# Optimization experiments

Measured on AMD Instinct MI355X. Metric: run time of the kernel, lower is better.

Reference implementation:

```python
import jax, jax.numpy as jnp
import numpy as np


def setup_inputs() -> dict:
    key = jax.random.key(0)
    k1, k2 = jax.random.split(key)
    x = jax.random.normal(k1, (8, 8192, 512), dtype=jnp.float32)
    codebook = jax.random.normal(k2, (1024, 512), dtype=jnp.float32)
    return {"x": x, "codebook": codebook}


def reference(x, codebook):
    # torch.cdist -> Euclidean distance; argmin is invariant under sqrt, so
    x2 = jnp.sum(x * x, axis=-1, keepdims=True)          # [B, N, 1]
    c2 = jnp.sum(codebook * codebook, axis=-1)           # [K]
    xc = jnp.einsum('bnd,kd->bnk', x, codebook)          # [B, N, K]
    d2 = x2 - 2.0 * xc + c2                              # [B, N, K]
    idx = jnp.argmin(d2, axis=-1)                        # [B, N]
    return codebook[idx]                                 # [B, N, dim]
```

## Files before the change

kernel.cpp:

```cpp
#include <hip/hip_runtime.h>
#include <cstdio>


typedef float f32x4 __attribute__((ext_vector_type(4)));
typedef _Float16 half8 __attribute__((ext_vector_type(8)));

#define KDIM 512
#define NCODES 1024
#define NQ 65536
#define TAU_S 0.05f

#define WS_XH    0ull
#define WS_CBH   67108864ull
#define WS_C2H   68157440ull
#define WS_C2D   68161536ull
#define WS_CAND1 68169728ull
#define WS_CBT   WS_CAND1
#define WS_CAND2 70266880ull
#define WS_CANDC 72364032ull
#define WS_IDX   74461184ull
#define WS_LIST  74723328ull
#define WS_CTR   74985472ull
#define WS_NEED  (WS_CTR + 4ull)

__device__ __forceinline__ unsigned short f2h(float f) {
  _Float16 h = (_Float16)f;
  return __builtin_bit_cast(unsigned short, h);
}

__device__ __forceinline__ void async16(const void* g, void* l) {
  __builtin_amdgcn_global_load_lds(
      (const __attribute__((address_space(1))) void*)g,
      (__attribute__((address_space(3))) void*)l, 16, 0, 0);
}

__global__ __launch_bounds__(256) void vq_prep(const float* __restrict__ cb,
                                               unsigned short* __restrict__ cbh,
                                               float* __restrict__ c2h,
                                               double* __restrict__ c2d) {
  int lane = threadIdx.x & 63;
  int row = blockIdx.x * 4 + (threadIdx.x >> 6);
  const float4* src = (const float4*)(cb + (size_t)row * KDIM);
  float4 u = src[lane * 2], v = src[lane * 2 + 1];
  double p = (double)u.x * u.x + (double)u.y * u.y + (double)u.z * u.z + (double)u.w * u.w +
             (double)v.x * v.x + (double)v.y * v.y + (double)v.z * v.z + (double)v.w * v.w;
#pragma unroll
  for (int m = 1; m < 64; m <<= 1) p += __shfl_xor(p, m);
  if (lane == 0) { c2h[row] = (float)(0.5 * p); c2d[row] = 0.5 * p; }
  unsigned r0 = f2h(u.x) | ((unsigned)f2h(u.y) << 16);
  unsigned r1 = f2h(u.z) | ((unsigned)f2h(u.w) << 16);
  unsigned r2 = f2h(v.x) | ((unsigned)f2h(v.y) << 16);
  unsigned r3 = f2h(v.z) | ((unsigned)f2h(v.w) << 16);
  *(int4*)(cbh + (size_t)row * KDIM + lane * 8) = make_int4((int)r0, (int)r1, (int)r2, (int)r3);
}

__global__ __launch_bounds__(256) void vq_convx(const float4* __restrict__ x4,
                                                int4* __restrict__ xh4) {
  size_t t = (size_t)blockIdx.x * 256 + threadIdx.x;
  float4 u = x4[t * 2], v = x4[t * 2 + 1];
  unsigned r0 = f2h(u.x) | ((unsigned)f2h(u.y) << 16);
  unsigned r1 = f2h(u.z) | ((unsigned)f2h(u.w) << 16);
  unsigned r2 = f2h(v.x) | ((unsigned)f2h(v.y) << 16);
  unsigned r3 = f2h(v.z) | ((unsigned)f2h(v.w) << 16);
  xh4[t] = make_int4((int)r0, (int)r1, (int)r2, (int)r3);
}

__global__ __launch_bounds__(256) void vq_main(const unsigned short* __restrict__ xh,
                                               const unsigned short* __restrict__ cbh,
                                               const float* __restrict__ c2h,
                                               float* __restrict__ cand1,
                                               float* __restrict__ cand2,
                                               int* __restrict__ candc) {
  __shared__ unsigned short As[2][128 * 32];
  __shared__ unsigned short Bs[2][128 * 32];
  __shared__ float red1[256], red2[256];
  __shared__ int redc[256];

  const int tid = threadIdx.x;
  const int lane = tid & 63, wv = tid >> 6;
  const int mw = wv & 1, nw = wv >> 1;
  const int c = lane & 15, q = lane >> 4;
  const int mb = blockIdx.x >> 3, nb = blockIdx.x & 7;

  const int r0 = tid >> 2, g0 = tid & 3;
  const int s0 = (r0 >> 1) & 3;
  const size_t xrow0 = (size_t)(mb * 128 + r0) * KDIM + ((g0 ^ s0) * 8);
  const size_t crow0 = (size_t)(nb * 128 + r0) * KDIM + ((g0 ^ s0) * 8);

  f32x4 acc[4][4];
#pragma unroll
  for (int i = 0; i < 4; ++i)
#pragma unroll
    for (int j = 0; j < 4; ++j) acc[i][j] = (f32x4){0.f, 0.f, 0.f, 0.f};

  async16(xh + xrow0,              &As[0][tid * 8]);
  async16(xh + xrow0 + 64 * KDIM,  &As[0][2048 + tid * 8]);
  async16(cbh + crow0,             &Bs[0][tid * 8]);
  async16(cbh + crow0 + 64 * KDIM, &Bs[0][2048 + tid * 8]);

  for (int ko = 0; ko < 16; ++ko) {
    const int cur = ko & 1;
    __syncthreads();
    if (ko + 1 < 16) {
      const int k0 = (ko + 1) * 32;
      async16(xh + xrow0 + k0,              &As[1 - cur][tid * 8]);
      async16(xh + xrow0 + 64 * KDIM + k0,  &As[1 - cur][2048 + tid * 8]);
      async16(cbh + crow0 + k0,             &Bs[1 - cur][tid * 8]);
      async16(cbh + crow0 + 64 * KDIM + k0, &Bs[1 - cur][2048 + tid * 8]);
    }
    half8 a[4], b[4];
#pragma unroll
    for (int i = 0; i < 4; ++i) {
      int mr = mw * 64 + i * 16 + c;
      a[i] = *(const half8*)&As[cur][mr * 32 + ((q ^ ((mr >> 1) & 3)) * 8)];
    }
#pragma unroll
    for (int j = 0; j < 4; ++j) {
      int nr = nw * 64 + j * 16 + c;
      b[j] = *(const half8*)&Bs[cur][nr * 32 + ((q ^ ((nr >> 1) & 3)) * 8)];
    }
#pragma unroll
    for (int i = 0; i < 4; ++i)
#pragma unroll
      for (int j = 0; j < 4; ++j)
        acc[i][j] = __builtin_amdgcn_mfma_f32_16x16x32_f16(a[i], b[j], acc[i][j], 0, 0, 0);
    __syncthreads();
  }

  float mn1[4][4], mn2[4][4];
  int mcol[4][4];
#pragma unroll
  for (int i = 0; i < 4; ++i)
#pragma unroll
    for (int r = 0; r < 4; ++r) { mn1[i][r] = 1e30f; mn2[i][r] = 1e30f; mcol[i][r] = 0; }
#pragma unroll
  for (int j = 0; j < 4; ++j) {
    int colb = nb * 128 + nw * 64 + j * 16 + c;
    float c2v = c2h[colb];
#pragma unroll
    for (int i = 0; i < 4; ++i)
#pragma unroll
      for (int r = 0; r < 4; ++r) {
        float sv = c2v - acc[i][j][r];
        float hi = fmaxf(sv, mn1[i][r]);
        mn2[i][r] = fminf(mn2[i][r], hi);
        bool lt = sv < mn1[i][r];
        mn1[i][r] = lt ? sv : mn1[i][r];
        mcol[i][r] = lt ? colb : mcol[i][r];
      }
  }
#pragma unroll
  for (int m = 1; m < 16; m <<= 1) {
#pragma unroll
    for (int i = 0; i < 4; ++i)
#pragma unroll
      for (int r = 0; r < 4; ++r) {
        float o1 = __shfl_xor(mn1[i][r], m);
        float o2 = __shfl_xor(mn2[i][r], m);
        int   oc = __shfl_xor(mcol[i][r], m);
        float hi = fmaxf(o1, mn1[i][r]);
        mn2[i][r] = fminf(fminf(mn2[i][r], o2), hi);
        bool lt = o1 < mn1[i][r];
        mn1[i][r] = lt ? o1 : mn1[i][r];
        mcol[i][r] = lt ? oc : mcol[i][r];
      }
  }
  if (c == 0) {
#pragma unroll
    for (int i = 0; i < 4; ++i)
#pragma unroll
      for (int r = 0; r < 4; ++r) {
        int rb = mw * 64 + i * 16 + q * 4 + r;
        red1[rb * 2 + nw] = mn1[i][r];
        red2[rb * 2 + nw] = mn2[i][r];
        redc[rb * 2 + nw] = mcol[i][r];
      }
  }
  __syncthreads();
  if (tid < 128) {
    float b1 = red1[tid * 2], b2 = red2[tid * 2];
    int bc = redc[tid * 2];
    float o1 = red1[tid * 2 + 1], o2 = red2[tid * 2 + 1];
    int oc = redc[tid * 2 + 1];
    float hi = fmaxf(o1, b1);
    b2 = fminf(fminf(b2, o2), hi);
    if (o1 < b1) { b1 = o1; bc = oc; }
    size_t qg = (size_t)(mb * 128 + tid) * 8 + nb;
    cand1[qg] = b1; cand2[qg] = b2; candc[qg] = bc;
  }
}

__global__ __launch_bounds__(256) void vq_reduce(const float4* __restrict__ c1,
                                                 const float4* __restrict__ c2,
                                                 const int4* __restrict__ cc,
                                                 int* __restrict__ idx,
                                                 int* __restrict__ list,
                                                 int* __restrict__ counter) {
  int qg = blockIdx.x * 256 + threadIdx.x;
  float4 a1 = c1[qg * 2], b1v = c1[qg * 2 + 1];
  float4 a2 = c2[qg * 2], b2v = c2[qg * 2 + 1];
  int4 ai = cc[qg * 2], bi = cc[qg * 2 + 1];
  float m1[8] = {a1.x, a1.y, a1.z, a1.w, b1v.x, b1v.y, b1v.z, b1v.w};
  float m2[8] = {a2.x, a2.y, a2.z, a2.w, b2v.x, b2v.y, b2v.z, b2v.w};
  int mc[8] = {ai.x, ai.y, ai.z, ai.w, bi.x, bi.y, bi.z, bi.w};
  float g1 = m1[0], g2 = m2[0];
  int gc = mc[0];
#pragma unroll
  for (int k = 1; k < 8; ++k) {
    float hi = fmaxf(m1[k], g1);
    g2 = fminf(fminf(g2, m2[k]), hi);
    if (m1[k] < g1) { g1 = m1[k]; gc = mc[k]; }
  }
  idx[qg] = gc;
  if (g2 - g1 < TAU_S) { int p = atomicAdd(counter, 1); list[p] = qg; }
}

__global__ __launch_bounds__(256) void vq_trans(const float4* __restrict__ cb4,
                                                float4* __restrict__ cbT4) {
  __shared__ float t[64][65];
  const int bc = blockIdx.x >> 3, bk = blockIdx.x & 7;
  const int c0 = bc * 64, k0 = bk * 64;
  const int r = threadIdx.x >> 4, q4 = threadIdx.x & 15;
#pragma unroll
  for (int p = 0; p < 4; ++p) {
    int row = p * 16 + r;
    float4 v = cb4[(size_t)(c0 + row) * 128 + (k0 >> 2) + q4];
    t[row][q4 * 4 + 0] = v.x; t[row][q4 * 4 + 1] = v.y;
    t[row][q4 * 4 + 2] = v.z; t[row][q4 * 4 + 3] = v.w;
  }
  __syncthreads();
#pragma unroll
  for (int p = 0; p < 4; ++p) {
    int kk = p * 16 + r;
    float4 v = make_float4(t[q4 * 4 + 0][kk], t[q4 * 4 + 1][kk],
                           t[q4 * 4 + 2][kk], t[q4 * 4 + 3][kk]);
    cbT4[(size_t)(k0 + kk) * 256 + (c0 >> 2) + q4] = v;
  }
}

__global__ __launch_bounds__(256) void vq_refine(const float* __restrict__ x,
                                                 const float4* __restrict__ cbT4,
                                                 const double* __restrict__ c2d,
                                                 const int* __restrict__ list,
                                                 const int* __restrict__ counter,
                                                 int* __restrict__ idx) {
  __shared__ float xs[512];
  __shared__ double rv[4];
  __shared__ int rc[4];
  const int cnt = counter[0];
  const int tid = threadIdx.x, lane = tid & 63, wv = tid >> 6;
  for (int qi = blockIdx.x; qi < cnt; qi += gridDim.x) {
    const int query = list[qi];
    __syncthreads();
    xs[tid] = x[(size_t)query * KDIM + tid];
    xs[tid + 256] = x[(size_t)query * KDIM + tid + 256];
    __syncthreads();
    double a0 = 0, a1 = 0, a2 = 0, a3 = 0;
    const float4* xs4 = (const float4*)xs;
#pragma unroll 2
    for (int k4 = 0; k4 < 128; ++k4) {
      float4 xv = xs4[k4];
      float4 c0 = cbT4[(k4 * 4 + 0) * 256 + tid];
      float4 c1 = cbT4[(k4 * 4 + 1) * 256 + tid];
      float4 c2v = cbT4[(k4 * 4 + 2) * 256 + tid];
      float4 c3 = cbT4[(k4 * 4 + 3) * 256 + tid];
      a0 = fma((double)xv.x, (double)c0.x, a0);
      a1 = fma((double)xv.x, (double)c0.y, a1);
      a2 = fma((double)xv.x, (double)c0.z, a2);
      a3 = fma((double)xv.x, (double)c0.w, a3);
      a0 = fma((double)xv.y, (double)c1.x, a0);
      a1 = fma((double)xv.y, (double)c1.y, a1);
      a2 = fma((double)xv.y, (double)c1.z, a2);
      a3 = fma((double)xv.y, (double)c1.w, a3);
      a0 = fma((double)xv.z, (double)c2v.x, a0);
      a1 = fma((double)xv.z, (double)c2v.y, a1);
      a2 = fma((double)xv.z, (double)c2v.z, a2);
      a3 = fma((double)xv.z, (double)c2v.w, a3);
      a0 = fma((double)xv.w, (double)c3.x, a0);
      a1 = fma((double)xv.w, (double)c3.y, a1);
      a2 = fma((double)xv.w, (double)c3.z, a2);
      a3 = fma((double)xv.w, (double)c3.w, a3);
    }
    double best = c2d[tid * 4] - a0;
    int bc = tid * 4;
    double s1 = c2d[tid * 4 + 1] - a1;
    if (s1 < best) { best = s1; bc = tid * 4 + 1; }
    double s2 = c2d[tid * 4 + 2] - a2;
    if (s2 < best) { best = s2; bc = tid * 4 + 2; }
    double s3 = c2d[tid * 4 + 3] - a3;
    if (s3 < best) { best = s3; bc = tid * 4 + 3; }
#pragma unroll
    for (int m = 1; m < 64; m <<= 1) {
      double o = __shfl_xor(best, m);
      int oc = __shfl_xor(bc, m);
      if (o < best) { best = o; bc = oc; }
    }
    if (lane == 0) { rv[wv] = best; rc[wv] = bc; }
    __syncthreads();
    if (tid == 0) {
      double b = rv[0]; int bci = rc[0];
#pragma unroll
      for (int w = 1; w < 4; ++w)
        if (rv[w] < b) { b = rv[w]; bci = rc[w]; }
      idx[query] = bci;
    }
    __syncthreads();
  }
}

__global__ __launch_bounds__(256) void vq_gather(const float* __restrict__ cb,
                                                 const int* __restrict__ idx,
                                                 float* __restrict__ out) {
  size_t i = (size_t)blockIdx.x * 256 + threadIdx.x;
  int qg = (int)(i >> 7), d = (int)(i & 127);
  ((float4*)out)[i] = ((const float4*)cb)[(size_t)idx[qg] * 128 + d];
}

extern "C" void kernel_launch(void* const* d_in, const int* in_sizes, int n_in,
                              void* d_out, int out_size, void* d_ws, size_t ws_size,
                              hipStream_t stream) {
  const float* x = (const float*)d_in[0];
  const float* cb = (const float*)d_in[1];
  float* out = (float*)d_out;
  char* ws = (char*)d_ws;
  if (ws_size < WS_NEED) {
    fprintf(stderr, "vq: ws_size %zu too small (need %llu)\n", ws_size,
            (unsigned long long)WS_NEED);
    return;
  }
  unsigned short* xh = (unsigned short*)(ws + WS_XH);
  unsigned short* cbh = (unsigned short*)(ws + WS_CBH);
  float* c2h = (float*)(ws + WS_C2H);
  double* c2d = (double*)(ws + WS_C2D);
  float* cand1 = (float*)(ws + WS_CAND1);
  float* cand2 = (float*)(ws + WS_CAND2);
  int* candc = (int*)(ws + WS_CANDC);
  float* cbT = (float*)(ws + WS_CBT);
  int* idx = (int*)(ws + WS_IDX);
  int* list = (int*)(ws + WS_LIST);
  int* counter = (int*)(ws + WS_CTR);

  hipMemsetAsync(counter, 0, 4, stream);
  vq_prep<<<256, 256, 0, stream>>>(cb, cbh, c2h, c2d);
  vq_convx<<<16384, 256, 0, stream>>>((const float4*)x, (int4*)xh);
  vq_main<<<4096, 256, 0, stream>>>(xh, cbh, c2h, cand1, cand2, candc);
  vq_reduce<<<256, 256, 0, stream>>>((const float4*)cand1, (const float4*)cand2,
                                     (const int4*)candc, idx, list, counter);
  vq_trans<<<128, 256, 0, stream>>>((const float4*)cb, (float4*)cbT);
  vq_refine<<<1024, 256, 0, stream>>>(x, (const float4*)cbT, c2d, list, counter, idx);
  vq_gather<<<32768, 256, 0, stream>>>(cb, idx, out);
}
```

Measured before the change: 435.9 us.

## Enlarge distance GEMM block tile to 256x256 with 16 waves

The main fp16 MFMA distance kernel now uses 1024-thread blocks that each cover a 256x256 query-by-code tile instead of 128x128. Each k-slice staged in LDS is therefore reused by more MFMAs, which cuts global and LDS traffic per FLOP. The trailing barrier in the double-buffered loop is dropped, and the reduction scratch aliases the staging pool. Because each query now yields four per-block candidate partials instead of eight, the candidate reduce kernel and the workspace offsets shrink to match. The refine kernel also gets a larger unroll and twice the grid. The cost is higher register and LDS pressure per block (64 KB pool, launch bound capping VGPRs), which may lower occupancy or cause spills.

```diff
diff --git a/kernel.cpp b/kernel.cpp
--- a/kernel.cpp
+++ b/kernel.cpp
@@ -16,11 +16,11 @@
 #define WS_C2D   68161536ull
 #define WS_CAND1 68169728ull
 #define WS_CBT   WS_CAND1
-#define WS_CAND2 70266880ull
-#define WS_CANDC 72364032ull
-#define WS_IDX   74461184ull
-#define WS_LIST  74723328ull
-#define WS_CTR   74985472ull
+#define WS_CAND2 69218304ull
+#define WS_CANDC 70266880ull
+#define WS_IDX   71315456ull
+#define WS_LIST  71577600ull
+#define WS_CTR   71839744ull
 #define WS_NEED  (WS_CTR + 4ull)
 
 __device__ __forceinline__ unsigned short f2h(float f) {
@@ -65,27 +65,29 @@
   xh4[t] = make_int4((int)r0, (int)r1, (int)r2, (int)r3);
 }
 
-__global__ __launch_bounds__(256) void vq_main(const unsigned short* __restrict__ xh,
-                                               const unsigned short* __restrict__ cbh,
-                                               const float* __restrict__ c2h,
-                                               float* __restrict__ cand1,
-                                               float* __restrict__ cand2,
-                                               int* __restrict__ candc) {
-  __shared__ unsigned short As[2][128 * 32];
-  __shared__ unsigned short Bs[2][128 * 32];
-  __shared__ float red1[256], red2[256];
-  __shared__ int redc[256];
+__global__ __launch_bounds__(1024, 4) void vq_main(const unsigned short* __restrict__ xh,
+                                                   const unsigned short* __restrict__ cbh,
+                                                   const float* __restrict__ c2h,
+                                                   float* __restrict__ cand1,
+                                                   float* __restrict__ cand2,
+                                                   int* __restrict__ candc) {
+  __shared__ char pool[65536];
+  unsigned short* As0 = (unsigned short*)pool;
+  unsigned short* Bs0 = (unsigned short*)(pool + 32768);
+  float* red1 = (float*)pool;
+  float* red2 = (float*)(pool + 4096);
+  int*   redc = (int*)(pool + 8192);
 
   const int tid = threadIdx.x;
   const int lane = tid & 63, wv = tid >> 6;
-  const int mw = wv & 1, nw = wv >> 1;
+  const int mw = wv & 3, nw = wv >> 2;
   const int c = lane & 15, q = lane >> 4;
-  const int mb = blockIdx.x >> 3, nb = blockIdx.x & 7;
+  const int mb = blockIdx.x >> 2, nb = blockIdx.x & 3;
 
   const int r0 = tid >> 2, g0 = tid & 3;
   const int s0 = (r0 >> 1) & 3;
-  const size_t xrow0 = (size_t)(mb * 128 + r0) * KDIM + ((g0 ^ s0) * 8);
-  const size_t crow0 = (size_t)(nb * 128 + r0) * KDIM + ((g0 ^ s0) * 8);
+  const size_t xrow0 = (size_t)(mb * 256 + r0) * KDIM + ((g0 ^ s0) * 8);
+  const size_t crow0 = (size_t)(nb * 256 + r0) * KDIM + ((g0 ^ s0) * 8);
 
   f32x4 acc[4][4];
 #pragma unroll
@@ -93,38 +95,35 @@
 #pragma unroll
     for (int j = 0; j < 4; ++j) acc[i][j] = (f32x4){0.f, 0.f, 0.f, 0.f};
 
-  async16(xh + xrow0,              &As[0][tid * 8]);
-  async16(xh + xrow0 + 64 * KDIM,  &As[0][2048 + tid * 8]);
-  async16(cbh + crow0,             &Bs[0][tid * 8]);
-  async16(cbh + crow0 + 64 * KDIM, &Bs[0][2048 + tid * 8]);
+  async16(xh + xrow0,  &As0[tid * 8]);
+  async16(cbh + crow0, &Bs0[tid * 8]);
 
   for (int ko = 0; ko < 16; ++ko) {
     const int cur = ko & 1;
     __syncthreads();
     if (ko + 1 < 16) {
       const int k0 = (ko + 1) * 32;
-      async16(xh + xrow0 + k0,              &As[1 - cur][tid * 8]);
-      async16(xh + xrow0 + 64 * KDIM + k0,  &As[1 - cur][2048 + tid * 8]);
-      async16(cbh + crow0 + k0,             &Bs[1 - cur][tid * 8]);
-      async16(cbh + crow0 + 64 * KDIM + k0, &Bs[1 - cur][2048 + tid * 8]);
-    }
+      async16(xh + xrow0 + k0,  &As0[(1 - cur) * 8192 + tid * 8]);
+      async16(cbh + crow0 + k0, &Bs0[(1 - cur) * 8192 + tid * 8]);
+    }
+    const unsigned short* A = &As0[cur * 8192];
+    const unsigned short* B = &Bs0[cur * 8192];
     half8 a[4], b[4];
 #pragma unroll
     for (int i = 0; i < 4; ++i) {
       int mr = mw * 64 + i * 16 + c;
-      a[i] = *(const half8*)&As[cur][mr * 32 + ((q ^ ((mr >> 1) & 3)) * 8)];
+      a[i] = *(const half8*)&A[mr * 32 + ((q ^ ((mr >> 1) & 3)) * 8)];
     }
 #pragma unroll
     for (int j = 0; j < 4; ++j) {
       int nr = nw * 64 + j * 16 + c;
-      b[j] = *(const half8*)&Bs[cur][nr * 32 + ((q ^ ((nr >> 1) & 3)) * 8)];
+      b[j] = *(const half8*)&B[nr * 32 + ((q ^ ((nr >> 1) & 3)) * 8)];
     }
 #pragma unroll
     for (int i = 0; i < 4; ++i)
 #pragma unroll
       for (int j = 0; j < 4; ++j)
         acc[i][j] = __builtin_amdgcn_mfma_f32_16x16x32_f16(a[i], b[j], acc[i][j], 0, 0, 0);
-    __syncthreads();
   }
 
   float mn1[4][4], mn2[4][4];
@@ -135,7 +134,7 @@
     for (int r = 0; r < 4; ++r) { mn1[i][r] = 1e30f; mn2[i][r] = 1e30f; mcol[i][r] = 0; }
 #pragma unroll
   for (int j = 0; j < 4; ++j) {
-    int colb = nb * 128 + nw * 64 + j * 16 + c;
+    int colb = nb * 256 + nw * 64 + j * 16 + c;
     float c2v = c2h[colb];
 #pragma unroll
     for (int i = 0; i < 4; ++i)
@@ -171,21 +170,24 @@
 #pragma unroll
       for (int r = 0; r < 4; ++r) {
         int rb = mw * 64 + i * 16 + q * 4 + r;
-        red1[rb * 2 + nw] = mn1[i][r];
-        red2[rb * 2 + nw] = mn2[i][r];
-        redc[rb * 2 + nw] = mcol[i][r];
+        red1[rb * 4 + nw] = mn1[i][r];
+        red2[rb * 4 + nw] = mn2[i][r];
+        redc[rb * 4 + nw] = mcol[i][r];
       }
   }
   __syncthreads();
-  if (tid < 128) {
-    float b1 = red1[tid * 2], b2 = red2[tid * 2];
-    int bc = redc[tid * 2];
-    float o1 = red1[tid * 2 + 1], o2 = red2[tid * 2 + 1];
-    int oc = redc[tid * 2 + 1];
-    float hi = fmaxf(o1, b1);
-    b2 = fminf(fminf(b2, o2), hi);
-    if (o1 < b1) { b1 = o1; bc = oc; }
-    size_t qg = (size_t)(mb * 128 + tid) * 8 + nb;
+  if (tid < 256) {
+    float b1 = red1[tid * 4], b2 = red2[tid * 4];
+    int bc = redc[tid * 4];
+#pragma unroll
+    for (int w = 1; w < 4; ++w) {
+      float o1 = red1[tid * 4 + w], o2 = red2[tid * 4 + w];
+      int oc = redc[tid * 4 + w];
+      float hi = fmaxf(o1, b1);
+      b2 = fminf(fminf(b2, o2), hi);
+      if (o1 < b1) { b1 = o1; bc = oc; }
+    }
+    size_t qg = (size_t)(mb * 256 + tid) * 4 + nb;
     cand1[qg] = b1; cand2[qg] = b2; candc[qg] = bc;
   }
 }
@@ -197,16 +199,16 @@
                                                  int* __restrict__ list,
                                                  int* __restrict__ counter) {
   int qg = blockIdx.x * 256 + threadIdx.x;
-  float4 a1 = c1[qg * 2], b1v = c1[qg * 2 + 1];
-  float4 a2 = c2[qg * 2], b2v = c2[qg * 2 + 1];
-  int4 ai = cc[qg * 2], bi = cc[qg * 2 + 1];
-  float m1[8] = {a1.x, a1.y, a1.z, a1.w, b1v.x, b1v.y, b1v.z, b1v.w};
-  float m2[8] = {a2.x, a2.y, a2.z, a2.w, b2v.x, b2v.y, b2v.z, b2v.w};
-  int mc[8] = {ai.x, ai.y, ai.z, ai.w, bi.x, bi.y, bi.z, bi.w};
+  float4 a1 = c1[qg];
+  float4 a2 = c2[qg];
+  int4 ai = cc[qg];
+  float m1[4] = {a1.x, a1.y, a1.z, a1.w};
+  float m2[4] = {a2.x, a2.y, a2.z, a2.w};
+  int mc[4] = {ai.x, ai.y, ai.z, ai.w};
   float g1 = m1[0], g2 = m2[0];
   int gc = mc[0];
 #pragma unroll
-  for (int k = 1; k < 8; ++k) {
+  for (int k = 1; k < 4; ++k) {
     float hi = fmaxf(m1[k], g1);
     g2 = fminf(fminf(g2, m2[k]), hi);
     if (m1[k] < g1) { g1 = m1[k]; gc = mc[k]; }
@@ -257,7 +259,7 @@
     __syncthreads();
     double a0 = 0, a1 = 0, a2 = 0, a3 = 0;
     const float4* xs4 = (const float4*)xs;
-#pragma unroll 2
+#pragma unroll 4
     for (int k4 = 0; k4 < 128; ++k4) {
       float4 xv = xs4[k4];
       float4 c0 = cbT4[(k4 * 4 + 0) * 256 + tid];
@@ -343,10 +345,10 @@
   hipMemsetAsync(counter, 0, 4, stream);
   vq_prep<<<256, 256, 0, stream>>>(cb, cbh, c2h, c2d);
   vq_convx<<<16384, 256, 0, stream>>>((const float4*)x, (int4*)xh);
-  vq_main<<<4096, 256, 0, stream>>>(xh, cbh, c2h, cand1, cand2, candc);
+  vq_main<<<1024, 1024, 0, stream>>>(xh, cbh, c2h, cand1, cand2, candc);
   vq_reduce<<<256, 256, 0, stream>>>((const float4*)cand1, (const float4*)cand2,
                                      (const int4*)candc, idx, list, counter);
   vq_trans<<<128, 256, 0, stream>>>((const float4*)cb, (float4*)cbT);
-  vq_refine<<<1024, 256, 0, stream>>>(x, (const float4*)cbT, c2d, list, counter, idx);
+  vq_refine<<<2048, 256, 0, stream>>>(x, (const float4*)cbT, c2d, list, counter, idx);
   vq_gather<<<32768, 256, 0, stream>>>(cb, idx, out);
 }
```

Result: faster. 417.7 us (-4.2%).
